# Kernel tuning notes

Hardware: AMD Instinct MI355X
Metric: run time of the kernel (lower is better)

The kernel has to match this reference:

```python
import jax, jax.numpy as jnp
import numpy as np

B, M, R = 1024, 2048, 8192  # batch of states, metabolites, reactions
SPARSITY = 0.002            # ~4 nonzero substrates / products per reaction


def setup_inputs() -> dict:
    key = jax.random.key(0)
    k1, k2, k3, k4, k5, k6 = jax.random.split(key, 6)
    # concentrations must be strictly positive (log used in power-law eval)
    conc = jax.random.uniform(k1, (B, M), minval=1e-3, maxval=1.0, dtype=jnp.float32)
    # sparse kinetic-order (exponent) matrix: ~4 substrates/reaction, order 1 or 2
    e_mask = jax.random.bernoulli(k2, SPARSITY, (M, R))
    E = jnp.where(e_mask, jax.random.randint(k3, (M, R), 1, 3), 0).astype(jnp.int32)
    # sparse stoichiometry matrix with coefficients in {-2,-1,1,2}
    s_mask = jax.random.bernoulli(k4, SPARSITY, (M, R))
    s_raw = jax.random.randint(k5, (M, R), 0, 4)
    s_val = jnp.where(s_raw < 2, s_raw - 2, s_raw - 1)  # {-2,-1,1,2}
    S = jnp.where(s_mask, s_val, 0).astype(jnp.int32)
    # per-reaction rate constants (the learned ParameterDict)
    k = jax.random.uniform(k6, (R,), minval=0.1, maxval=2.0, dtype=jnp.float32)
    return {"conc": conc, "E": E, "S": S, "k": k}


def reference(conc, E, S, k):
    # mass-action rate laws: v_j = k_j * prod_i c_i^{E_ij}, evaluated in log-space
    # logc: [B, M]; Ef: [M, R] -> v: [B, R]
    logc = jnp.log(conc)
    Ef = E.astype(conc.dtype)
    v = k * jnp.exp(jnp.einsum('bm,mr->br', logc, Ef))
    # stoichiometric ODE RHS: dX/dt = v @ S^T -> [B, M]
    Sf = S.astype(conc.dtype)
    dXdt = jnp.einsum('br,mr->bm', v, Sf)
    return dXdt
```

## Files before the change

kernel.cpp:

```cpp
#include <hip/hip_runtime.h>
#include <hip/hip_fp16.h>

#define Bsz 1024
#define Mm  2048
#define Rr  8192
#define EMAX 32
#define SMAX 64

typedef unsigned short ushort_t;

__global__ __launch_bounds__(256) void transpose_log(
    const float* __restrict__ conc, __half2* __restrict__ logcTh2,
    int* __restrict__ ecnt, unsigned int* __restrict__ elist32)
{
    const int g = blockIdx.x * 256 + threadIdx.x;
    if (g < Rr) ecnt[g] = 0;
    elist32[g] = 0;

    __shared__ float tile[64][65];
    const int mt = (blockIdx.x % (Mm / 64)) * 64;
    const int bt = (blockIdx.x / (Mm / 64)) * 64;
    const int lm = threadIdx.x & 63;
    const int w  = threadIdx.x >> 6;
    for (int i = w; i < 64; i += 4)
        tile[lm][i] = __logf(conc[(size_t)(bt + i) * Mm + mt + lm]);
    __syncthreads();
    const int s       = bt >> 7;
    const int colbase = (bt & 127) >> 1;
    __half2* dst = logcTh2 + (size_t)s * (Mm * 64);
    for (int idx = threadIdx.x; idx < 64 * 32; idx += 256) {
        const int j  = idx >> 5;
        const int bp = idx & 31;
        dst[(mt + j) * 64 + colbase + bp] =
            __floats2half2_rn(tile[j][2 * bp], tile[j][2 * bp + 1]);
    }
}

__global__ __launch_bounds__(256) void build_lists(
    const int* __restrict__ E, const int* __restrict__ S,
    int* __restrict__ ecnt, ushort_t* __restrict__ elist,
    int* __restrict__ scnt, ushort_t* __restrict__ slist)
{
    __shared__ int n_hits;
    __shared__ int buf[256];
    const int t = threadIdx.x;
    if (t == 0) n_hits = 0;
    __syncthreads();

    if (blockIdx.x < 2048) {
        const int m = blockIdx.x;
        const int4* E4 = (const int4*)E + (size_t)m * 2048;
        int4 e[8];
        #pragma unroll
        for (int u = 0; u < 8; ++u) e[u] = E4[t + 256 * u];
        #pragma unroll
        for (int u = 0; u < 8; ++u) {
            const int r0 = (t + 256 * u) << 2;
            int ev[4] = {e[u].x, e[u].y, e[u].z, e[u].w};
            #pragma unroll
            for (int q = 0; q < 4; ++q)
                if (ev[q]) {
                    int i = atomicAdd(&n_hits, 1);
                    if (i < 256) buf[i] = (ev[q] << 13) | (r0 + q);
                }
        }
        __syncthreads();
        const int en = min(n_hits, 256);
        if (t < en) {
            int wv = buf[t];
            int r  = wv & 0x1FFF;
            int ev = wv >> 13;
            int slot = atomicAdd(&ecnt[r], 1);
            if (slot < EMAX) elist[r * EMAX + slot] = (ushort_t)((ev << 11) | m);
        }
    } else {
        const int m = blockIdx.x - 2048;
        const int4* S4 = (const int4*)S + (size_t)m * 2048;
        int4 s[8];
        #pragma unroll
        for (int u = 0; u < 8; ++u) s[u] = S4[t + 256 * u];
        #pragma unroll
        for (int u = 0; u < 8; ++u) {
            const int r0 = (t + 256 * u) << 2;
            int sv[4] = {s[u].x, s[u].y, s[u].z, s[u].w};
            #pragma unroll
            for (int q = 0; q < 4; ++q)
                if (sv[q]) {
                    int i = atomicAdd(&n_hits, 1);
                    if (i < 256) buf[i] = ((sv[q] + 2) << 13) | (r0 + q);
                }
        }
        __syncthreads();
        const int sn = min(n_hits, SMAX);
        if (t == 0) scnt[m] = sn;
        if (t < SMAX)
            slist[m * SMAX + t] = (t < sn) ? (ushort_t)buf[t]
                                           : (ushort_t)0x4000;
    }
}

__global__ __launch_bounds__(256) void rates_kernel(
    const __half2* __restrict__ logcTh2, const float* __restrict__ kvec,
    const int* __restrict__ ecnt, const ushort_t* __restrict__ elist,
    __half2* __restrict__ VTh)
{
    const int s   = blockIdx.x & 7;
    const int rch = blockIdx.x >> 3;
    const int col = threadIdx.x & 63;
    const int wr  = threadIdx.x >> 6;
    const __half2* lc = logcTh2 + (size_t)s * (Mm * 64);
    __half2* vt = VTh + (size_t)s * (Rr * 64);
    unsigned w; float2 g;
    #define EGATHER(word)                                                  \
        w = (unsigned)(word);                                              \
        g = __half22float2(lc[(w & 0x7FF) * 64 + col]);                    \
        acc.x += (float)((w & 0xFFFF) >> 11) * g.x;                        \
        acc.y += (float)((w & 0xFFFF) >> 11) * g.y;                        \
        g = __half22float2(lc[((w >> 16) & 0x7FF) * 64 + col]);            \
        acc.x += (float)(w >> 27) * g.x;                                   \
        acc.y += (float)(w >> 27) * g.y;
    for (int i = 0; i < 8; ++i) {
        const int r = rch * 32 + i * 4 + wr;
        const ushort_t* row = elist + (r << 5);
        float2 acc = make_float2(0.f, 0.f);
        int2 W = *(const int2*)(row);
        EGATHER(W.x) EGATHER(W.y)
        const int cnt = min(ecnt[r], EMAX);
        for (int j = 4; j < cnt; j += 4) {
            int2 T = *(const int2*)(row + j);
            EGATHER(T.x) EGATHER(T.y)
        }
        const float kk = kvec[r];
        vt[r * 64 + col] = __floats2half2_rn(kk * __expf(acc.x), kk * __expf(acc.y));
    }
    #undef EGATHER
}

__global__ __launch_bounds__(256) void assemble_kernel(
    const __half2* __restrict__ VTh, const int* __restrict__ scnt,
    const ushort_t* __restrict__ slist, float* __restrict__ out)
{
    __shared__ float tile[128][17];
    const int s   = blockIdx.x & 7;
    const int mch = blockIdx.x >> 3;
    const int col = threadIdx.x & 63;
    const int wm  = threadIdx.x >> 6;
    const __half2* vt = VTh + (size_t)s * (Rr * 64);
    const int m0 = mch * 16;
    unsigned w; float2 v; float sw;
    #define SGATHER(word)                                                  \
        w = (unsigned)(word);                                              \
        v = __half22float2(vt[(w & 0x1FFF) * 64 + col]);                   \
        sw = (float)((int)((w & 0xFFFF) >> 13) - 2);                       \
        a.x += sw * v.x;  a.y += sw * v.y;                                 \
        v = __half22float2(vt[((w >> 16) & 0x1FFF) * 64 + col]);           \
        sw = (float)((int)(w >> 29) - 2);                                  \
        a.x += sw * v.x;  a.y += sw * v.y;
    for (int i = 0; i < 4; ++i) {
        const int ml = i * 4 + wm;
        const int m  = m0 + ml;
        const ushort_t* row = slist + (m << 6);
        float2 a = make_float2(0.f, 0.f);
        int4 W0 = *(const int4*)(row);
        int4 W1 = *(const int4*)(row + 8);
        SGATHER(W0.x) SGATHER(W0.y) SGATHER(W0.z) SGATHER(W0.w)
        SGATHER(W1.x) SGATHER(W1.y) SGATHER(W1.z) SGATHER(W1.w)
        const int cnt = min(scnt[m], SMAX);
        for (int j = 16; j < cnt; j += 8) {
            int4 T = *(const int4*)(row + j);
            SGATHER(T.x) SGATHER(T.y) SGATHER(T.z) SGATHER(T.w)
        }
        tile[2 * col][ml]     = a.x;
        tile[2 * col + 1][ml] = a.y;
    }
    #undef SGATHER
    __syncthreads();
    #pragma unroll
    for (int pass = 0; pass < 2; ++pass) {
        const int bl = (threadIdx.x >> 2) + pass * 64;
        const int fl = threadIdx.x & 3;
        float4 vv = *(const float4*)&tile[bl][fl * 4];
        *(float4*)(out + (size_t)(s * 128 + bl) * Mm + m0 + fl * 4) = vv;
    }
}

extern "C" void kernel_launch(void* const* d_in, const int* in_sizes, int n_in,
                              void* d_out, int out_size, void* d_ws, size_t ws_size,
                              hipStream_t stream) {
    const float* conc = (const float*)d_in[0];
    const int*   E    = (const int*)d_in[1];
    const int*   S    = (const int*)d_in[2];
    const float* kvec = (const float*)d_in[3];
    float* out = (float*)d_out;

    __half2* VTh     = (__half2*)d_ws;
    __half2* logcTh2 = (__half2*)((char*)d_ws + (size_t)Rr * Bsz * sizeof(__half));
    int*    ecnt     = (int*)((char*)logcTh2 + (size_t)Mm * Bsz * sizeof(__half));
    int*    scnt     = ecnt + Rr;
    ushort_t* elist  = (ushort_t*)(scnt + Mm);
    ushort_t* slist  = elist + Rr * EMAX;
    const size_t need = (size_t)Rr * Bsz * sizeof(__half)
                      + (size_t)Mm * Bsz * sizeof(__half)
                      + (size_t)(Rr + Mm) * sizeof(int)
                      + (size_t)(Rr * EMAX + Mm * SMAX) * sizeof(ushort_t);
    if (ws_size < need) return;

    transpose_log<<<512, 256, 0, stream>>>(conc, logcTh2, ecnt, (unsigned int*)elist);
    build_lists<<<4096, 256, 0, stream>>>(E, S, ecnt, elist, scnt, slist);
    rates_kernel<<<2048, 256, 0, stream>>>(logcTh2, kvec, ecnt, elist, VTh);
    assemble_kernel<<<1024, 256, 0, stream>>>(VTh, scnt, slist, out);
}
```

Before: 193.1 us.

## Fuse rate evaluation into stoichiometric assembly, dropping the VTh intermediate

Merges the rates and assemble kernels. Each metabolite's output now recomputes the rate of every reaction in its stoichiometry list directly from the log-concentration gathers. This removes writing and re-reading the half-precision rate matrix and one kernel launch. In exchange, each reaction rate (gathers plus exp) is recomputed once per metabolite that references it, multiplying that work.

```diff
diff --git a/kernel.cpp b/kernel.cpp
--- a/kernel.cpp
+++ b/kernel.cpp
@@ -99,19 +99,22 @@
     }
 }
 
-__global__ __launch_bounds__(256) void rates_kernel(
+__global__ __launch_bounds__(256) void fused_out(
     const __half2* __restrict__ logcTh2, const float* __restrict__ kvec,
     const int* __restrict__ ecnt, const ushort_t* __restrict__ elist,
-    __half2* __restrict__ VTh)
+    const int* __restrict__ scnt, const ushort_t* __restrict__ slist,
+    float* __restrict__ out)
 {
+    __shared__ float tile[8][130];
     const int s   = blockIdx.x & 7;
-    const int rch = blockIdx.x >> 3;
+    const int mch = blockIdx.x >> 3;
     const int col = threadIdx.x & 63;
-    const int wr  = threadIdx.x >> 6;
+    const int wm  = threadIdx.x >> 6;
     const __half2* lc = logcTh2 + (size_t)s * (Mm * 64);
-    __half2* vt = VTh + (size_t)s * (Rr * 64);
+    const int m0 = mch * 8;
+
     unsigned w; float2 g;
-    #define EGATHER(word)                                                  \
+    #define EG(word, acc)                                                  \
         w = (unsigned)(word);                                              \
         g = __half22float2(lc[(w & 0x7FF) * 64 + col]);                    \
         acc.x += (float)((w & 0xFFFF) >> 11) * g.x;                        \
@@ -119,69 +122,51 @@
         g = __half22float2(lc[((w >> 16) & 0x7FF) * 64 + col]);            \
         acc.x += (float)(w >> 27) * g.x;                                   \
         acc.y += (float)(w >> 27) * g.y;
-    for (int i = 0; i < 8; ++i) {
-        const int r = rch * 32 + i * 4 + wr;
-        const ushort_t* row = elist + (r << 5);
-        float2 acc = make_float2(0.f, 0.f);
-        int2 W = *(const int2*)(row);
-        EGATHER(W.x) EGATHER(W.y)
-        const int cnt = min(ecnt[r], EMAX);
-        for (int j = 4; j < cnt; j += 4) {
-            int2 T = *(const int2*)(row + j);
-            EGATHER(T.x) EGATHER(T.y)
-        }
-        const float kk = kvec[r];
-        vt[r * 64 + col] = __floats2half2_rn(kk * __expf(acc.x), kk * __expf(acc.y));
-    }
-    #undef EGATHER
-}
 
-__global__ __launch_bounds__(256) void assemble_kernel(
-    const __half2* __restrict__ VTh, const int* __restrict__ scnt,
-    const ushort_t* __restrict__ slist, float* __restrict__ out)
-{
-    __shared__ float tile[128][17];
-    const int s   = blockIdx.x & 7;
-    const int mch = blockIdx.x >> 3;
-    const int col = threadIdx.x & 63;
-    const int wm  = threadIdx.x >> 6;
-    const __half2* vt = VTh + (size_t)s * (Rr * 64);
-    const int m0 = mch * 16;
-    unsigned w; float2 v; float sw;
-    #define SGATHER(word)                                                  \
-        w = (unsigned)(word);                                              \
-        v = __half22float2(vt[(w & 0x1FFF) * 64 + col]);                   \
-        sw = (float)((int)((w & 0xFFFF) >> 13) - 2);                       \
-        a.x += sw * v.x;  a.y += sw * v.y;                                 \
-        v = __half22float2(vt[((w >> 16) & 0x1FFF) * 64 + col]);           \
-        sw = (float)((int)(w >> 29) - 2);                                  \
-        a.x += sw * v.x;  a.y += sw * v.y;
-    for (int i = 0; i < 4; ++i) {
+    for (int i = 0; i < 2; ++i) {
         const int ml = i * 4 + wm;
         const int m  = m0 + ml;
-        const ushort_t* row = slist + (m << 6);
+        const ushort_t* srow = slist + (m << 6);
+        const int cnt = scnt[m];
         float2 a = make_float2(0.f, 0.f);
-        int4 W0 = *(const int4*)(row);
-        int4 W1 = *(const int4*)(row + 8);
-        SGATHER(W0.x) SGATHER(W0.y) SGATHER(W0.z) SGATHER(W0.w)
-        SGATHER(W1.x) SGATHER(W1.y) SGATHER(W1.z) SGATHER(W1.w)
-        const int cnt = min(scnt[m], SMAX);
-        for (int j = 16; j < cnt; j += 8) {
-            int4 T = *(const int4*)(row + j);
-            SGATHER(T.x) SGATHER(T.y) SGATHER(T.z) SGATHER(T.w)
+        unsigned pr = *(const unsigned*)(srow);
+        for (int j = 0; j < cnt; j += 2) {
+            const unsigned cur = pr;
+            if (j + 2 < cnt) pr = *(const unsigned*)(srow + j + 2);
+            const unsigned eA = cur & 0xFFFFu, eB = cur >> 16;
+            const int   rA  = eA & 0x1FFF,  rB  = eB & 0x1FFF;
+            const float swA = (float)((int)(eA >> 13) - 2);
+            const float swB = (float)((int)(eB >> 13) - 2);
+            const ushort_t* erA = elist + (rA << 5);
+            const ushort_t* erB = elist + (rB << 5);
+            const int ceA = ecnt[rA], ceB = ecnt[rB];
+            const float kA = kvec[rA], kB = kvec[rB];
+            int2 GA = *(const int2*)erA;
+            int2 GB = *(const int2*)erB;
+            float2 lgA = make_float2(0.f, 0.f), lgB = make_float2(0.f, 0.f);
+            EG(GA.x, lgA) EG(GA.y, lgA)
+            EG(GB.x, lgB) EG(GB.y, lgB)
+            for (int tt = 4; tt < ceA; tt += 4) {
+                int2 T = *(const int2*)(erA + tt);
+                EG(T.x, lgA) EG(T.y, lgA)
+            }
+            for (int tt = 4; tt < ceB; tt += 4) {
+                int2 T = *(const int2*)(erB + tt);
+                EG(T.x, lgB) EG(T.y, lgB)
+            }
+            a.x += swA * kA * __expf(lgA.x) + swB * kB * __expf(lgB.x);
+            a.y += swA * kA * __expf(lgA.y) + swB * kB * __expf(lgB.y);
         }
-        tile[2 * col][ml]     = a.x;
-        tile[2 * col + 1][ml] = a.y;
+        tile[ml][2 * col]     = a.x;
+        tile[ml][2 * col + 1] = a.y;
     }
-    #undef SGATHER
+    #undef EG
     __syncthreads();
-    #pragma unroll
-    for (int pass = 0; pass < 2; ++pass) {
-        const int bl = (threadIdx.x >> 2) + pass * 64;
-        const int fl = threadIdx.x & 3;
-        float4 vv = *(const float4*)&tile[bl][fl * 4];
-        *(float4*)(out + (size_t)(s * 128 + bl) * Mm + m0 + fl * 4) = vv;
-    }
+    const int bl = threadIdx.x >> 1;
+    const int fl = (threadIdx.x & 1) * 4;
+    float4 vv = make_float4(tile[fl + 0][bl], tile[fl + 1][bl],
+                            tile[fl + 2][bl], tile[fl + 3][bl]);
+    *(float4*)(out + (size_t)(s * 128 + bl) * Mm + m0 + fl) = vv;
 }
 
 extern "C" void kernel_launch(void* const* d_in, const int* in_sizes, int n_in,
@@ -193,20 +178,17 @@
     const float* kvec = (const float*)d_in[3];
     float* out = (float*)d_out;
 
-    __half2* VTh     = (__half2*)d_ws;
-    __half2* logcTh2 = (__half2*)((char*)d_ws + (size_t)Rr * Bsz * sizeof(__half));
-    int*    ecnt     = (int*)((char*)logcTh2 + (size_t)Mm * Bsz * sizeof(__half));
+    __half2* logcTh2 = (__half2*)d_ws;
+    int*    ecnt     = (int*)((char*)d_ws + (size_t)Mm * Bsz * sizeof(__half));
     int*    scnt     = ecnt + Rr;
     ushort_t* elist  = (ushort_t*)(scnt + Mm);
     ushort_t* slist  = elist + Rr * EMAX;
-    const size_t need = (size_t)Rr * Bsz * sizeof(__half)
-                      + (size_t)Mm * Bsz * sizeof(__half)
+    const size_t need = (size_t)Mm * Bsz * sizeof(__half)
                       + (size_t)(Rr + Mm) * sizeof(int)
                       + (size_t)(Rr * EMAX + Mm * SMAX) * sizeof(ushort_t);
     if (ws_size < need) return;
 
     transpose_log<<<512, 256, 0, stream>>>(conc, logcTh2, ecnt, (unsigned int*)elist);
     build_lists<<<4096, 256, 0, stream>>>(E, S, ecnt, elist, scnt, slist);
-    rates_kernel<<<2048, 256, 0, stream>>>(logcTh2, kvec, ecnt, elist, VTh);
-    assemble_kernel<<<1024, 256, 0, stream>>>(VTh, scnt, slist, out);
+    fused_out<<<2048, 256, 0, stream>>>(logcTh2, kvec, ecnt, elist, scnt, slist, out);
 }
```

Result: slower. 208.9 us (+8.2%).

## Merge prep kernels, drop elist zeroing, and batch list loads in gather kernels

Applied to the files above, without the earlier changes.

The log-transpose and list-building kernels become one prep kernel, and a tiny kernel zeroes only the counters. The old zeroing of the exponent list is removed; out-of-range entries are masked by per-row counts instead. The rates and assemble kernels now preload counts, list words and rate constants for several rows per wave before gathering. This raises memory-level parallelism and makes the row index wave-uniform via readfirstlane. The cost is higher register pressure, and unclamped counts rely on rows staying under the list capacity.

```diff
diff --git a/kernel.cpp b/kernel.cpp
--- a/kernel.cpp
+++ b/kernel.cpp
@@ -9,85 +9,54 @@
 
 typedef unsigned short ushort_t;
 
-__global__ __launch_bounds__(256) void transpose_log(
-    const float* __restrict__ conc, __half2* __restrict__ logcTh2,
-    int* __restrict__ ecnt, unsigned int* __restrict__ elist32)
-{
-    const int g = blockIdx.x * 256 + threadIdx.x;
-    if (g < Rr) ecnt[g] = 0;
-    elist32[g] = 0;
-
-    __shared__ float tile[64][65];
-    const int mt = (blockIdx.x % (Mm / 64)) * 64;
-    const int bt = (blockIdx.x / (Mm / 64)) * 64;
-    const int lm = threadIdx.x & 63;
-    const int w  = threadIdx.x >> 6;
-    for (int i = w; i < 64; i += 4)
-        tile[lm][i] = __logf(conc[(size_t)(bt + i) * Mm + mt + lm]);
-    __syncthreads();
-    const int s       = bt >> 7;
-    const int colbase = (bt & 127) >> 1;
-    __half2* dst = logcTh2 + (size_t)s * (Mm * 64);
-    for (int idx = threadIdx.x; idx < 64 * 32; idx += 256) {
-        const int j  = idx >> 5;
-        const int bp = idx & 31;
-        dst[(mt + j) * 64 + colbase + bp] =
-            __floats2half2_rn(tile[j][2 * bp], tile[j][2 * bp + 1]);
-    }
-}
-
-__global__ __launch_bounds__(256) void build_lists(
-    const int* __restrict__ E, const int* __restrict__ S,
-    int* __restrict__ ecnt, ushort_t* __restrict__ elist,
+__global__ __launch_bounds__(256) void zero_ecnt(int* __restrict__ p) {
+    p[blockIdx.x * 256 + threadIdx.x] = 0;
+}
+
+__global__ __launch_bounds__(256) void prep_kernel(
+    const float* __restrict__ conc, const int* __restrict__ E, const int* __restrict__ S,
+    __half2* __restrict__ logcTh2, int* __restrict__ ecnt, ushort_t* __restrict__ elist,
     int* __restrict__ scnt, ushort_t* __restrict__ slist)
 {
+    __shared__ float tile[64][65];
     __shared__ int n_hits;
     __shared__ int buf[256];
-    const int t = threadIdx.x;
-    if (t == 0) n_hits = 0;
-    __syncthreads();
-
-    if (blockIdx.x < 2048) {
-        const int m = blockIdx.x;
-        const int4* E4 = (const int4*)E + (size_t)m * 2048;
-        int4 e[8];
-        #pragma unroll
-        for (int u = 0; u < 8; ++u) e[u] = E4[t + 256 * u];
+    const int bid = blockIdx.x;
+    const int t   = threadIdx.x;
+
+    if (bid < 512) {
+        const int mt = (bid & 31) * 64;
+        const int bt = (bid >> 5) * 64;
+        const int lm = t & 63;
+        const int w  = t >> 6;
+        for (int i = w; i < 64; i += 4)
+            tile[lm][i] = __logf(conc[(size_t)(bt + i) * Mm + mt + lm]);
+        __syncthreads();
+        const int s       = bt >> 7;
+        const int colbase = (bt & 127) >> 1;
+        __half2* dst = logcTh2 + (size_t)s * (Mm * 64);
+        for (int idx = t; idx < 64 * 32; idx += 256) {
+            const int j = idx >> 5, bp = idx & 31;
+            dst[(mt + j) * 64 + colbase + bp] =
+                __floats2half2_rn(tile[j][2 * bp], tile[j][2 * bp + 1]);
+        }
+    } else if (bid < 2560) {
+        const int m = bid - 512;
+        if (t == 0) n_hits = 0;
+        __syncthreads();
+        const int4* S4 = (const int4*)S + (size_t)m * 2048;
+        int4 sv[8];
+        #pragma unroll
+        for (int u = 0; u < 8; ++u) sv[u] = S4[t + 256 * u];
         #pragma unroll
         for (int u = 0; u < 8; ++u) {
             const int r0 = (t + 256 * u) << 2;
-            int ev[4] = {e[u].x, e[u].y, e[u].z, e[u].w};
+            int v[4] = {sv[u].x, sv[u].y, sv[u].z, sv[u].w};
             #pragma unroll
             for (int q = 0; q < 4; ++q)
-                if (ev[q]) {
+                if (v[q]) {
                     int i = atomicAdd(&n_hits, 1);
-                    if (i < 256) buf[i] = (ev[q] << 13) | (r0 + q);
-                }
-        }
-        __syncthreads();
-        const int en = min(n_hits, 256);
-        if (t < en) {
-            int wv = buf[t];
-            int r  = wv & 0x1FFF;
-            int ev = wv >> 13;
-            int slot = atomicAdd(&ecnt[r], 1);
-            if (slot < EMAX) elist[r * EMAX + slot] = (ushort_t)((ev << 11) | m);
-        }
-    } else {
-        const int m = blockIdx.x - 2048;
-        const int4* S4 = (const int4*)S + (size_t)m * 2048;
-        int4 s[8];
-        #pragma unroll
-        for (int u = 0; u < 8; ++u) s[u] = S4[t + 256 * u];
-        #pragma unroll
-        for (int u = 0; u < 8; ++u) {
-            const int r0 = (t + 256 * u) << 2;
-            int sv[4] = {s[u].x, s[u].y, s[u].z, s[u].w};
-            #pragma unroll
-            for (int q = 0; q < 4; ++q)
-                if (sv[q]) {
-                    int i = atomicAdd(&n_hits, 1);
-                    if (i < 256) buf[i] = ((sv[q] + 2) << 13) | (r0 + q);
+                    if (i < 256) buf[i] = ((v[q] + 2) << 13) | (r0 + q);
                 }
         }
         __syncthreads();
@@ -96,6 +65,34 @@
         if (t < SMAX)
             slist[m * SMAX + t] = (t < sn) ? (ushort_t)buf[t]
                                            : (ushort_t)0x4000;
+    } else {
+        const int m = bid - 2560;
+        if (t == 0) n_hits = 0;
+        __syncthreads();
+        const int4* E4 = (const int4*)E + (size_t)m * 2048;
+        int4 ev[8];
+        #pragma unroll
+        for (int u = 0; u < 8; ++u) ev[u] = E4[t + 256 * u];
+        #pragma unroll
+        for (int u = 0; u < 8; ++u) {
+            const int r0 = (t + 256 * u) << 2;
+            int v[4] = {ev[u].x, ev[u].y, ev[u].z, ev[u].w};
+            #pragma unroll
+            for (int q = 0; q < 4; ++q)
+                if (v[q]) {
+                    int i = atomicAdd(&n_hits, 1);
+                    if (i < 256) buf[i] = (v[q] << 13) | (r0 + q);
+                }
+        }
+        __syncthreads();
+        const int en = min(n_hits, 256);
+        if (t < en) {
+            int wv = buf[t];
+            int r  = wv & 0x1FFF;
+            int e  = wv >> 13;
+            int slot = atomicAdd(&ecnt[r], 1);
+            if (slot < EMAX) elist[r * EMAX + slot] = (ushort_t)((e << 11) | m);
+        }
     }
 }
 
@@ -107,33 +104,48 @@
     const int s   = blockIdx.x & 7;
     const int rch = blockIdx.x >> 3;
     const int col = threadIdx.x & 63;
-    const int wr  = threadIdx.x >> 6;
+    const int wr  = __builtin_amdgcn_readfirstlane(threadIdx.x >> 6);
     const __half2* lc = logcTh2 + (size_t)s * (Mm * 64);
     __half2* vt = VTh + (size_t)s * (Rr * 64);
-    unsigned w; float2 g;
-    #define EGATHER(word)                                                  \
-        w = (unsigned)(word);                                              \
-        g = __half22float2(lc[(w & 0x7FF) * 64 + col]);                    \
-        acc.x += (float)((w & 0xFFFF) >> 11) * g.x;                        \
-        acc.y += (float)((w & 0xFFFF) >> 11) * g.y;                        \
-        g = __half22float2(lc[((w >> 16) & 0x7FF) * 64 + col]);            \
-        acc.x += (float)(w >> 27) * g.x;                                   \
-        acc.y += (float)(w >> 27) * g.y;
+    const int rb = rch * 32 + wr * 8;
+
+    int  cnt[8]; int2 L0[8]; float kk[8];
+    #pragma unroll
     for (int i = 0; i < 8; ++i) {
-        const int r = rch * 32 + i * 4 + wr;
-        const ushort_t* row = elist + (r << 5);
-        float2 acc = make_float2(0.f, 0.f);
-        int2 W = *(const int2*)(row);
-        EGATHER(W.x) EGATHER(W.y)
-        const int cnt = min(ecnt[r], EMAX);
-        for (int j = 4; j < cnt; j += 4) {
-            int2 T = *(const int2*)(row + j);
-            EGATHER(T.x) EGATHER(T.y)
-        }
-        const float kk = kvec[r];
-        vt[r * 64 + col] = __floats2half2_rn(kk * __expf(acc.x), kk * __expf(acc.y));
-    }
-    #undef EGATHER
+        const int r = rb + i;
+        cnt[i] = ecnt[r];
+        L0[i]  = *(const int2*)(elist + (r << 5));
+        kk[i]  = kvec[r];
+    }
+    float2 acc[8];
+    unsigned w; float2 g; float v0, v1;
+    #define EG2(word, c0, c1, A)                                               \
+        w = (unsigned)(word);                                                  \
+        v0 = (c0) ? (float)((w & 0xFFFF) >> 11) : 0.f;                         \
+        v1 = (c1) ? (float)(w >> 27) : 0.f;                                    \
+        g = __half22float2(lc[(w & 0x7FF) * 64 + col]);                        \
+        A.x += v0 * g.x;  A.y += v0 * g.y;                                     \
+        g = __half22float2(lc[((w >> 16) & 0x7FF) * 64 + col]);                \
+        A.x += v1 * g.x;  A.y += v1 * g.y;
+    #pragma unroll
+    for (int i = 0; i < 8; ++i) {
+        acc[i] = make_float2(0.f, 0.f);
+        EG2(L0[i].x, cnt[i] > 0, cnt[i] > 1, acc[i])
+        EG2(L0[i].y, cnt[i] > 2, cnt[i] > 3, acc[i])
+    }
+    #pragma unroll
+    for (int i = 0; i < 8; ++i) {
+        for (int j = 4; j < cnt[i]; j += 4) {
+            int2 T = *(const int2*)(elist + ((rb + i) << 5) + j);
+            EG2(T.x, j + 0 < cnt[i], j + 1 < cnt[i], acc[i])
+            EG2(T.y, j + 2 < cnt[i], j + 3 < cnt[i], acc[i])
+        }
+    }
+    #undef EG2
+    #pragma unroll
+    for (int i = 0; i < 8; ++i)
+        vt[(rb + i) * 64 + col] =
+            __floats2half2_rn(kk[i] * __expf(acc[i].x), kk[i] * __expf(acc[i].y));
 }
 
 __global__ __launch_bounds__(256) void assemble_kernel(
@@ -144,36 +156,41 @@
     const int s   = blockIdx.x & 7;
     const int mch = blockIdx.x >> 3;
     const int col = threadIdx.x & 63;
-    const int wm  = threadIdx.x >> 6;
+    const int wm  = __builtin_amdgcn_readfirstlane(threadIdx.x >> 6);
     const __half2* vt = VTh + (size_t)s * (Rr * 64);
     const int m0 = mch * 16;
+
+    int scn[4]; int4 W0[4], W1[4];
+    #pragma unroll
+    for (int i = 0; i < 4; ++i) {
+        const int m = m0 + i * 4 + wm;
+        scn[i] = scnt[m];
+        W0[i]  = *(const int4*)(slist + (m << 6));
+        W1[i]  = *(const int4*)(slist + (m << 6) + 8);
+    }
     unsigned w; float2 v; float sw;
-    #define SGATHER(word)                                                  \
-        w = (unsigned)(word);                                              \
-        v = __half22float2(vt[(w & 0x1FFF) * 64 + col]);                   \
-        sw = (float)((int)((w & 0xFFFF) >> 13) - 2);                       \
-        a.x += sw * v.x;  a.y += sw * v.y;                                 \
-        v = __half22float2(vt[((w >> 16) & 0x1FFF) * 64 + col]);           \
-        sw = (float)((int)(w >> 29) - 2);                                  \
-        a.x += sw * v.x;  a.y += sw * v.y;
+    #define SG(word, A)                                                        \
+        w = (unsigned)(word);                                                  \
+        v = __half22float2(vt[(w & 0x1FFF) * 64 + col]);                       \
+        sw = (float)((int)((w & 0xFFFF) >> 13) - 2);                           \
+        A.x += sw * v.x;  A.y += sw * v.y;                                     \
+        v = __half22float2(vt[((w >> 16) & 0x1FFF) * 64 + col]);               \
+        sw = (float)((int)(w >> 29) - 2);                                      \
+        A.x += sw * v.x;  A.y += sw * v.y;
+    #pragma unroll
     for (int i = 0; i < 4; ++i) {
         const int ml = i * 4 + wm;
-        const int m  = m0 + ml;
-        const ushort_t* row = slist + (m << 6);
         float2 a = make_float2(0.f, 0.f);
-        int4 W0 = *(const int4*)(row);
-        int4 W1 = *(const int4*)(row + 8);
-        SGATHER(W0.x) SGATHER(W0.y) SGATHER(W0.z) SGATHER(W0.w)
-        SGATHER(W1.x) SGATHER(W1.y) SGATHER(W1.z) SGATHER(W1.w)
-        const int cnt = min(scnt[m], SMAX);
-        for (int j = 16; j < cnt; j += 8) {
-            int4 T = *(const int4*)(row + j);
-            SGATHER(T.x) SGATHER(T.y) SGATHER(T.z) SGATHER(T.w)
+        SG(W0[i].x, a) SG(W0[i].y, a) SG(W0[i].z, a) SG(W0[i].w, a)
+        SG(W1[i].x, a) SG(W1[i].y, a) SG(W1[i].z, a) SG(W1[i].w, a)
+        for (int j = 16; j < scn[i]; j += 8) {
+            int4 T = *(const int4*)(slist + ((m0 + ml) << 6) + j);
+            SG(T.x, a) SG(T.y, a) SG(T.z, a) SG(T.w, a)
         }
         tile[2 * col][ml]     = a.x;
         tile[2 * col + 1][ml] = a.y;
     }
-    #undef SGATHER
+    #undef SG
     __syncthreads();
     #pragma unroll
     for (int pass = 0; pass < 2; ++pass) {
@@ -205,8 +222,8 @@
                       + (size_t)(Rr * EMAX + Mm * SMAX) * sizeof(ushort_t);
     if (ws_size < need) return;
 
-    transpose_log<<<512, 256, 0, stream>>>(conc, logcTh2, ecnt, (unsigned int*)elist);
-    build_lists<<<4096, 256, 0, stream>>>(E, S, ecnt, elist, scnt, slist);
+    zero_ecnt<<<32, 256, 0, stream>>>(ecnt);
+    prep_kernel<<<4608, 256, 0, stream>>>(conc, E, S, logcTh2, ecnt, elist, scnt, slist);
     rates_kernel<<<2048, 256, 0, stream>>>(logcTh2, kvec, ecnt, elist, VTh);
     assemble_kernel<<<1024, 256, 0, stream>>>(VTh, scnt, slist, out);
 }
```

After: 182.3 us. 5.6% less time.
